# Optimization experiments

Measured on AMD Instinct MI355X. Metric: run time of the kernel, lower is better.

The kernel has to match this reference:

```python
import jax, jax.numpy as jnp
import numpy as np

NUM_GRAPHS = 64
N, E, H = 100000, 3200000, 64


def _glorot(k, shape):
    fan_in = shape[0]
    return jax.random.normal(k, shape, jnp.float32) * (1.0 / np.sqrt(fan_in))


def setup_inputs() -> dict:
    key = jax.random.key(0)
    ks = jax.random.split(key, 16)
    edge_index = jax.random.randint(ks[0], (2, E), 0, N)
    edge_weight = jax.random.uniform(ks[1], (E,), dtype=jnp.float32)
    batch = jnp.sort(jax.random.randint(ks[2], (N,), 0, NUM_GRAPHS))
    return {
        "edge_index": edge_index,
        "edge_weight": edge_weight,
        "batch": batch,
        "num_nodes": N,
        "W1": _glorot(ks[3], (1, H)), "b1": jnp.zeros((H,), jnp.float32),
        "W2": _glorot(ks[4], (H, H)), "b2": jnp.zeros((H,), jnp.float32),
        "W3": _glorot(ks[5], (H, H)), "b3": jnp.zeros((H,), jnp.float32),
        "W4": _glorot(ks[6], (H, H)), "b4": jnp.zeros((H,), jnp.float32),
        "W5": _glorot(ks[7], (H, H)), "b5": jnp.zeros((H,), jnp.float32),
        "lin_w": _glorot(ks[8], (H, 1)), "lin_b": jnp.zeros((1,), jnp.float32),
    }


def _gcn_layer(x, W, b, src, dst, w, n):
    # GCNConv(normalize=False): linear transform then weighted scatter-add over edges.
    h = x @ W                                  # [N, H]
    m = h[src] * w[:, None]                    # [E, H] messages
    return jax.ops.segment_sum(m, dst, num_segments=n) + b


def reference(edge_index, edge_weight, batch, num_nodes,
              W1, b1, W2, b2, W3, b3, W4, b4, W5, b5, lin_w, lin_b):
    src, dst = edge_index[0], edge_index[1]
    x = jnp.ones((num_nodes, 1), jnp.float32)
    for W, b in ((W1, b1), (W2, b2), (W3, b3), (W4, b4), (W5, b5)):
        x = jax.nn.relu(_gcn_layer(x, W, b, src, dst, edge_weight, num_nodes))
        # dropout p=0.1 is identity in eval mode
    # global mean pool per graph
    sums = jax.ops.segment_sum(x, batch, num_segments=NUM_GRAPHS)      # [G, H]
    counts = jax.ops.segment_sum(jnp.ones((num_nodes,), x.dtype), batch,
                                 num_segments=NUM_GRAPHS)
    pooled = sums / jnp.maximum(counts, 1.0)[:, None]
    return pooled @ lin_w + lin_b                                      # [G, 1]
```

## Files before the change

kernel.cpp:

```cpp
#include <hip/hip_runtime.h>

#define H 64
#define NUM_GRAPHS 64
#define BSHIFT 8
#define BSIZE 256
#define MAXNB 512
#define CHUNK 8192
#define RPB 16

typedef unsigned int uint;
typedef unsigned short ushort;
typedef __attribute__((ext_vector_type(4))) float f32x4;
typedef __attribute__((ext_vector_type(8))) short short8;

__device__ __forceinline__ float bf2f(ushort u) {
    return __uint_as_float(((uint)u) << 16);
}
__device__ __forceinline__ ushort f2bf(float f) {
    uint b = __float_as_uint(f);
    b += 0x7FFFu + ((b >> 16) & 1u);
    return (ushort)(b >> 16);
}

__global__ __launch_bounds__(1024) void bhist_kernel(const int* __restrict__ dst,
        int* __restrict__ bucketCnt, int E, int NB) {
    __shared__ int h[MAXNB];
    int tid = threadIdx.x;
    for (int i = tid; i < NB; i += 1024) h[i] = 0;
    __syncthreads();
    int base = blockIdx.x * CHUNK;
    int end = min(base + CHUNK, E);
    for (int e = base + tid; e < end; e += 1024)
        atomicAdd(&h[dst[e] >> BSHIFT], 1);
    __syncthreads();
    for (int i = tid; i < NB; i += 1024)
        if (h[i]) atomicAdd(&bucketCnt[i], h[i]);
}

__global__ __launch_bounds__(MAXNB) void bscan_kernel(const int* __restrict__ bucketCnt,
        int* __restrict__ bucketPtr, int* __restrict__ bucketCur, int NB) {
    __shared__ int s[MAXNB];
    int tid = threadIdx.x;
    int v = (tid < NB) ? bucketCnt[tid] : 0;
    s[tid] = v;
    __syncthreads();
    for (int off = 1; off < MAXNB; off <<= 1) {
        int t = (tid >= off) ? s[tid - off] : 0;
        __syncthreads();
        s[tid] += t;
        __syncthreads();
    }
    if (tid < NB) {
        bucketPtr[tid + 1] = s[tid];
        bucketCur[tid] = s[tid] - v;
    }
    if (tid == 0) bucketPtr[0] = 0;
}

__global__ __launch_bounds__(1024) void part_kernel(const int* __restrict__ src,
        const int* __restrict__ dst, const float* __restrict__ w,
        int* __restrict__ bucketCur, int2* __restrict__ bucketed, int E, int NB) {
    __shared__ int h[MAXNB];
    __shared__ int basev[MAXNB];
    int tid = threadIdx.x;
    for (int i = tid; i < NB; i += 1024) h[i] = 0;
    __syncthreads();
    int cbase = blockIdx.x * CHUNK;
    int cend = min(cbase + CHUNK, E);
    for (int e = cbase + tid; e < cend; e += 1024)
        atomicAdd(&h[dst[e] >> BSHIFT], 1);
    __syncthreads();
    for (int i = tid; i < NB; i += 1024) {
        int c = h[i];
        basev[i] = c ? atomicAdd(&bucketCur[i], c) : 0;
    }
    __syncthreads();
    for (int i = tid; i < NB; i += 1024) h[i] = 0;
    __syncthreads();
    for (int e = cbase + tid; e < cend; e += 1024) {
        int d = dst[e];
        int b = d >> BSHIFT;
        int slot = atomicAdd(&h[b], 1);
        bucketed[basev[b] + slot] =
            make_int2(((d & (BSIZE - 1)) << 17) | src[e], __float_as_int(w[e]));
    }
}

__global__ __launch_bounds__(512) void bsort_kernel(const int* __restrict__ bucketPtr,
        const int2* __restrict__ bucketed, uint* __restrict__ csr,
        int* __restrict__ rowptr, int N, int E) {
    __shared__ int cnt[BSIZE];
    __shared__ int pos[BSIZE];
    int b = blockIdx.x;
    int tid = threadIdx.x;
    int nodeBase = b << BSHIFT;
    int nNodes = min(BSIZE, N - nodeBase);
    if (tid < BSIZE) cnt[tid] = 0;
    __syncthreads();
    int ebeg = bucketPtr[b], eend = bucketPtr[b + 1];
    for (int e = ebeg + tid; e < eend; e += 512)
        atomicAdd(&cnt[bucketed[e].x >> 17], 1);
    __syncthreads();
    if (tid < BSIZE) pos[tid] = cnt[tid];
    __syncthreads();
    for (int off = 1; off < BSIZE; off <<= 1) {
        int t = (tid < BSIZE && tid >= off) ? pos[tid - off] : 0;
        __syncthreads();
        if (tid < BSIZE) pos[tid] += t;
        __syncthreads();
    }
    if (tid < nNodes)
        rowptr[nodeBase + tid] = ebeg + pos[tid] - cnt[tid];
    if (b == 0 && tid == 0) rowptr[N] = E;
    __syncthreads();
    if (tid < BSIZE) cnt[tid] = pos[tid] - cnt[tid];
    __syncthreads();
    for (int e = ebeg + tid; e < eend; e += 512) {
        int2 v = bucketed[e];
        int slot = atomicAdd(&cnt[v.x >> 17], 1);
        uint wb = (uint)v.y;
        wb += 0x7FFFu + ((wb >> 16) & 1u);
        uint w15 = (wb >> 16) & 0x7FFFu;
        uint s   = (uint)(v.x & 0x1FFFF);
        csr[ebeg + slot] = (s << 15) | w15;
    }
}

__global__ void layer1_kernel(const int* __restrict__ rowptr, const uint* __restrict__ csr,
                              const float* __restrict__ W1, const float* __restrict__ b1,
                              ushort* __restrict__ out, int N) {
    int lane = threadIdx.x & 63, wid = threadIdx.x >> 6;
    int row = blockIdx.x * 4 + wid;
    if (row >= N) return;
    int beg = rowptr[row], end = rowptr[row + 1];
    float s = 0.f;
    for (int e = beg + lane; e < end; e += 64) {
        uint p = __builtin_nontemporal_load(csr + e);
        s += __uint_as_float((p & 0x7FFFu) << 16);
    }
#pragma unroll
    for (int off = 32; off; off >>= 1) s += __shfl_xor(s, off);
    float v = s * W1[lane] + b1[lane];
    __builtin_nontemporal_store(f2bf(fmaxf(v, 0.f)), out + (size_t)row * H + lane);
}

__global__ __launch_bounds__(256) void layer_kernel(const int* __restrict__ rowptr,
        const uint* __restrict__ csr, const ushort* __restrict__ x,
        const float* __restrict__ W, const float* __restrict__ b,
        ushort* __restrict__ out, int N) {
    __shared__ alignas(16) ushort Wt[64][72];
    __shared__ alignas(16) ushort AG[RPB][72];
    int tid = threadIdx.x;
    for (int i = tid; i < 64 * 64; i += 256) {
        int k = i >> 6, c = i & 63;
        Wt[c][k] = f2bf(W[i]);
    }
    __syncthreads();
    int lane = tid & 63, wid = tid >> 6;
    int rowbase = blockIdx.x * RPB;
    for (int p = 0; p < 4; ++p) {
        int trow = wid * 4 + p;
        int row = rowbase + trow;
        float agg = 0.f;
        if (row < N) {
            int beg = rowptr[row], end = rowptr[row + 1];
            int len = end - beg;
            for (int ck = 0; ck < len; ck += 64) {
                uint pv = 0u;
                int idx = beg + ck + lane;
                if (idx < end) pv = __builtin_nontemporal_load(csr + idx);
                int rem = len - ck;
                int grps = rem >= 64 ? 8 : ((rem + 7) >> 3);
#pragma unroll
                for (int g = 0; g < 8; ++g) {
                    if (g < grps) {
#pragma unroll
                        for (int j = 0; j < 8; ++j) {
                            uint s = (uint)__builtin_amdgcn_readlane((int)pv, g * 8 + j);
                            float wf = __uint_as_float((s & 0x7FFFu) << 16);
                            float xv = bf2f(x[((s >> 15) << 6) + (uint)lane]);
                            agg = fmaf(wf, xv, agg);
                        }
                    }
                }
            }
        }
        AG[trow][lane] = f2bf(agg);
    }
    __syncthreads();
    int c0 = wid * 16;
    int cl = lane & 15, kg = lane >> 4;
    short8 a0 = *reinterpret_cast<const short8*>(&AG[cl][kg * 8]);
    short8 a1 = *reinterpret_cast<const short8*>(&AG[cl][32 + kg * 8]);
    short8 bb0 = *reinterpret_cast<const short8*>(&Wt[c0 + cl][kg * 8]);
    short8 bb1 = *reinterpret_cast<const short8*>(&Wt[c0 + cl][32 + kg * 8]);
    f32x4 acc = {0.f, 0.f, 0.f, 0.f};
    acc = __builtin_amdgcn_mfma_f32_16x16x32_bf16(a0, bb0, acc, 0, 0, 0);
    acc = __builtin_amdgcn_mfma_f32_16x16x32_bf16(a1, bb1, acc, 0, 0, 0);
    float bias = b[c0 + cl];
#pragma unroll
    for (int j = 0; j < 4; ++j) {
        int r = rowbase + kg * 4 + j;
        if (r < N) {
            float v = fmaxf(acc[j] + bias, 0.f);
            __builtin_nontemporal_store(f2bf(v), out + (size_t)r * H + c0 + cl);
        }
    }
}

__global__ void pool_kernel(const ushort* __restrict__ x, const int* __restrict__ batch,
                            const float* __restrict__ linw, float* __restrict__ gsum,
                            float* __restrict__ gcnt, int N) {
    __shared__ float bins[NUM_GRAPHS];
    __shared__ float cnts[NUM_GRAPHS];
    int tid = threadIdx.x;
    if (tid < NUM_GRAPHS) { bins[tid] = 0.f; cnts[tid] = 0.f; }
    __syncthreads();
    int node = blockIdx.x * 256 + tid;
    if (node < N) {
        const uint4* xv = reinterpret_cast<const uint4*>(x + (size_t)node * H);
        float acc = 0.f;
#pragma unroll
        for (int k = 0; k < 8; ++k) {
            uint4 u = xv[k];
            int c = k * 8;
            acc += bf2f((ushort)(u.x & 0xFFFF)) * linw[c + 0]
                 + bf2f((ushort)(u.x >> 16))    * linw[c + 1]
                 + bf2f((ushort)(u.y & 0xFFFF)) * linw[c + 2]
                 + bf2f((ushort)(u.y >> 16))    * linw[c + 3]
                 + bf2f((ushort)(u.z & 0xFFFF)) * linw[c + 4]
                 + bf2f((ushort)(u.z >> 16))    * linw[c + 5]
                 + bf2f((ushort)(u.w & 0xFFFF)) * linw[c + 6]
                 + bf2f((ushort)(u.w >> 16))    * linw[c + 7];
        }
        int g = batch[node];
        atomicAdd(&bins[g], acc);
        atomicAdd(&cnts[g], 1.f);
    }
    __syncthreads();
    if (tid < NUM_GRAPHS) {
        if (bins[tid] != 0.f || cnts[tid] != 0.f) {
            unsafeAtomicAdd(&gsum[tid], bins[tid]);
            unsafeAtomicAdd(&gcnt[tid], cnts[tid]);
        }
    }
}

__global__ void final_kernel(const float* __restrict__ gsum, const float* __restrict__ gcnt,
                             const float* __restrict__ lin_b, float* __restrict__ out) {
    int g = threadIdx.x;
    if (g < NUM_GRAPHS) out[g] = gsum[g] / fmaxf(gcnt[g], 1.f) + lin_b[0];
}

extern "C" void kernel_launch(void* const* d_in, const int* in_sizes, int n_in,
                              void* d_out, int out_size, void* d_ws, size_t ws_size,
                              hipStream_t stream) {
    const int*   edge_index = (const int*)d_in[0];
    const float* ew    = (const float*)d_in[1];
    const int*   batch = (const int*)d_in[2];
    const float* W1    = (const float*)d_in[4];
    const float* b1    = (const float*)d_in[5];
    const float* Wl[4] = {(const float*)d_in[6], (const float*)d_in[8],
                          (const float*)d_in[10], (const float*)d_in[12]};
    const float* bl[4] = {(const float*)d_in[7], (const float*)d_in[9],
                          (const float*)d_in[11], (const float*)d_in[13]};
    const float* linw  = (const float*)d_in[14];
    const float* linb  = (const float*)d_in[15];

    const int E = in_sizes[1];
    const int N = in_sizes[2];
    const int* src = edge_index;
    const int* dst = edge_index + E;
    const int NB = (N + BSIZE - 1) >> BSHIFT;

    char* base = (char*)d_ws;
    uint* csr = (uint*)base;
    size_t csrBytes = (((size_t)E * 4) + 255) & ~(size_t)255;
    ushort* bufA = (ushort*)(base + csrBytes);
    size_t featBytes = (size_t)N * H * 2;
    ushort* bufB = bufA + (size_t)N * H;
    int2* bucketed = (int2*)bufA;
    size_t span = 2 * featBytes;
    size_t bktBytes = (size_t)E * 8;
    if (bktBytes > span) span = bktBytes;
    span = (span + 255) & ~(size_t)255;
    char* tail = base + csrBytes + span;
    int* rowptr    = (int*)tail;
    int* bucketCnt = rowptr + (N + 1);
    int* bucketPtr = bucketCnt + MAXNB;
    int* bucketCur = bucketPtr + MAXNB + 1;
    float* gsum    = (float*)(bucketCur + MAXNB);
    float* gcnt    = gsum + NUM_GRAPHS;

    const int chunks = (E + CHUNK - 1) / CHUNK;

    hipMemsetAsync(bucketCnt, 0, MAXNB * sizeof(int), stream);
    bhist_kernel<<<chunks, 1024, 0, stream>>>(dst, bucketCnt, E, NB);
    bscan_kernel<<<1, MAXNB, 0, stream>>>(bucketCnt, bucketPtr, bucketCur, NB);
    part_kernel<<<chunks, 1024, 0, stream>>>(src, dst, ew, bucketCur, bucketed, E, NB);
    bsort_kernel<<<NB, 512, 0, stream>>>(bucketPtr, bucketed, csr, rowptr, N, E);

    layer1_kernel<<<(N + 3) / 4, 256, 0, stream>>>(rowptr, csr, W1, b1, bufA, N);

    ushort* in = bufA;
    ushort* outb = bufB;
    for (int l = 0; l < 4; ++l) {
        layer_kernel<<<(N + RPB - 1) / RPB, 256, 0, stream>>>(rowptr, csr, in, Wl[l], bl[l], outb, N);
        ushort* t = in; in = outb; outb = t;
    }

    hipMemsetAsync(gsum, 0, 2 * NUM_GRAPHS * sizeof(float), stream);
    pool_kernel<<<(N + 255) / 256, 256, 0, stream>>>(in, batch, linw, gsum, gcnt, N);
    final_kernel<<<1, 64, 0, stream>>>(gsum, gcnt, linb, (float*)d_out);
}
```

Before: 417.6 us.

## Sort edges by source within rows, fold degree into sort, fuse pooling into last layer

The bucket sort now uses a composite key of destination and high source bits, so edges within each row are ordered by source for better gather locality. It also accumulates per-node weighted degree, which turns layer 1 into an elementwise kernel instead of a CSR pass. Layer kernels become persistent with a fixed grid looping over row chunks. The last layer folds the ReLU output times lin_w straight into per-graph sums, so the final feature write and the pool kernel go away. The costs are larger shared memory in the sort, a longer prefix scan, and shared atomics in the last layer.

After: 552.9 us. 1.32x slower.

```diff
diff --git a/kernel.cpp b/kernel.cpp
--- a/kernel.cpp
+++ b/kernel.cpp
@@ -7,6 +7,9 @@
 #define MAXNB 512
 #define CHUNK 8192
 #define RPB 16
+#define NSB 64
+#define KEYS (BSIZE * NSB)
+#define GRID_L 1024
 
 typedef unsigned int uint;
 typedef unsigned short ushort;
@@ -88,161 +91,161 @@
 
 __global__ __launch_bounds__(512) void bsort_kernel(const int* __restrict__ bucketPtr,
         const int2* __restrict__ bucketed, uint* __restrict__ csr,
-        int* __restrict__ rowptr, int N, int E) {
-    __shared__ int cnt[BSIZE];
-    __shared__ int pos[BSIZE];
+        int* __restrict__ rowptr, float* __restrict__ degw, int N, int E) {
+    __shared__ int cnt[KEYS];
+    __shared__ int parts[512];
+    __shared__ float wsum[BSIZE];
     int b = blockIdx.x;
     int tid = threadIdx.x;
     int nodeBase = b << BSHIFT;
     int nNodes = min(BSIZE, N - nodeBase);
-    if (tid < BSIZE) cnt[tid] = 0;
+    for (int i = tid; i < KEYS; i += 512) cnt[i] = 0;
+    if (tid < BSIZE) wsum[tid] = 0.f;
     __syncthreads();
     int ebeg = bucketPtr[b], eend = bucketPtr[b + 1];
-    for (int e = ebeg + tid; e < eend; e += 512)
-        atomicAdd(&cnt[bucketed[e].x >> 17], 1);
-    __syncthreads();
-    if (tid < BSIZE) pos[tid] = cnt[tid];
-    __syncthreads();
-    for (int off = 1; off < BSIZE; off <<= 1) {
-        int t = (tid < BSIZE && tid >= off) ? pos[tid - off] : 0;
-        __syncthreads();
-        if (tid < BSIZE) pos[tid] += t;
-        __syncthreads();
-    }
-    if (tid < nNodes)
-        rowptr[nodeBase + tid] = ebeg + pos[tid] - cnt[tid];
-    if (b == 0 && tid == 0) rowptr[N] = E;
-    __syncthreads();
-    if (tid < BSIZE) cnt[tid] = pos[tid] - cnt[tid];
-    __syncthreads();
     for (int e = ebeg + tid; e < eend; e += 512) {
         int2 v = bucketed[e];
-        int slot = atomicAdd(&cnt[v.x >> 17], 1);
+        int key = ((v.x >> 17) << 6) | ((int)(((uint)(v.x & 0x1FFFF)) >> 11));
+        atomicAdd(&cnt[key], 1);
+    }
+    __syncthreads();
+    int base = tid * 32;
+    int run = 0;
+#pragma unroll
+    for (int j = 0; j < 32; ++j) { int t = cnt[base + j]; cnt[base + j] = run; run += t; }
+    parts[tid] = run;
+    __syncthreads();
+    for (int off = 1; off < 512; off <<= 1) {
+        int t = (tid >= off) ? parts[tid - off] : 0;
+        __syncthreads();
+        parts[tid] += t;
+        __syncthreads();
+    }
+    int add = (tid > 0) ? parts[tid - 1] : 0;
+#pragma unroll
+    for (int j = 0; j < 32; ++j) cnt[base + j] += add;
+    __syncthreads();
+    if (tid < nNodes) rowptr[nodeBase + tid] = ebeg + cnt[tid << 6];
+    if (b == 0 && tid == 0) rowptr[N] = E;
+    __syncthreads();
+    for (int e = ebeg + tid; e < eend; e += 512) {
+        int2 v = bucketed[e];
+        int dl = v.x >> 17;
+        int key = (dl << 6) | ((int)(((uint)(v.x & 0x1FFFF)) >> 11));
+        int slot = atomicAdd(&cnt[key], 1);
         uint wb = (uint)v.y;
         wb += 0x7FFFu + ((wb >> 16) & 1u);
         uint w15 = (wb >> 16) & 0x7FFFu;
-        uint s   = (uint)(v.x & 0x1FFFF);
-        csr[ebeg + slot] = (s << 15) | w15;
-    }
-}
-
-__global__ void layer1_kernel(const int* __restrict__ rowptr, const uint* __restrict__ csr,
-                              const float* __restrict__ W1, const float* __restrict__ b1,
-                              ushort* __restrict__ out, int N) {
-    int lane = threadIdx.x & 63, wid = threadIdx.x >> 6;
-    int row = blockIdx.x * 4 + wid;
-    if (row >= N) return;
-    int beg = rowptr[row], end = rowptr[row + 1];
-    float s = 0.f;
-    for (int e = beg + lane; e < end; e += 64) {
-        uint p = __builtin_nontemporal_load(csr + e);
-        s += __uint_as_float((p & 0x7FFFu) << 16);
-    }
-#pragma unroll
-    for (int off = 32; off; off >>= 1) s += __shfl_xor(s, off);
-    float v = s * W1[lane] + b1[lane];
-    __builtin_nontemporal_store(f2bf(fmaxf(v, 0.f)), out + (size_t)row * H + lane);
-}
-
+        csr[ebeg + slot] = (((uint)(v.x & 0x1FFFF)) << 15) | w15;
+        atomicAdd(&wsum[dl], __uint_as_float(w15 << 16));
+    }
+    __syncthreads();
+    if (tid < nNodes) degw[nodeBase + tid] = wsum[tid];
+}
+
+__global__ void layer1_kernel(const float* __restrict__ degw, const float* __restrict__ W1,
+                              const float* __restrict__ b1, ushort* __restrict__ out, int N) {
+    int gid = blockIdx.x * 256 + threadIdx.x;
+    if (gid >= N * 16) return;
+    int i = gid >> 4, c4 = (gid & 15) * 4;
+    float d = degw[i];
+    uint lo = (uint)f2bf(fmaxf(d * W1[c4 + 0] + b1[c4 + 0], 0.f))
+            | ((uint)f2bf(fmaxf(d * W1[c4 + 1] + b1[c4 + 1], 0.f)) << 16);
+    uint hi = (uint)f2bf(fmaxf(d * W1[c4 + 2] + b1[c4 + 2], 0.f))
+            | ((uint)f2bf(fmaxf(d * W1[c4 + 3] + b1[c4 + 3], 0.f)) << 16);
+    uint2 v = make_uint2(lo, hi);
+    *reinterpret_cast<uint2*>(out + ((size_t)i << 6) + c4) = v;
+}
+
+__global__ void count_kernel(const int* __restrict__ batch, float* __restrict__ gcnt, int N) {
+    __shared__ int bins[NUM_GRAPHS];
+    int tid = threadIdx.x;
+    if (tid < NUM_GRAPHS) bins[tid] = 0;
+    __syncthreads();
+    int node = blockIdx.x * 256 + tid;
+    if (node < N) atomicAdd(&bins[batch[node]], 1);
+    __syncthreads();
+    if (tid < NUM_GRAPHS && bins[tid])
+        unsafeAtomicAdd(&gcnt[tid], (float)bins[tid]);
+}
+
+template<bool LAST>
 __global__ __launch_bounds__(256) void layer_kernel(const int* __restrict__ rowptr,
         const uint* __restrict__ csr, const ushort* __restrict__ x,
-        const float* __restrict__ W, const float* __restrict__ b,
-        ushort* __restrict__ out, int N) {
+        const float* __restrict__ W, const float* __restrict__ bvec,
+        ushort* __restrict__ out, const int* __restrict__ batch,
+        const float* __restrict__ linw, float* __restrict__ gsum,
+        int N, int nchunk) {
     __shared__ alignas(16) ushort Wt[64][72];
     __shared__ alignas(16) ushort AG[RPB][72];
+    __shared__ float gbins[NUM_GRAPHS];
     int tid = threadIdx.x;
     for (int i = tid; i < 64 * 64; i += 256) {
         int k = i >> 6, c = i & 63;
         Wt[c][k] = f2bf(W[i]);
     }
+    if (LAST && tid < NUM_GRAPHS) gbins[tid] = 0.f;
     __syncthreads();
     int lane = tid & 63, wid = tid >> 6;
-    int rowbase = blockIdx.x * RPB;
-    for (int p = 0; p < 4; ++p) {
-        int trow = wid * 4 + p;
-        int row = rowbase + trow;
-        float agg = 0.f;
-        if (row < N) {
-            int beg = rowptr[row], end = rowptr[row + 1];
-            int len = end - beg;
-            for (int ck = 0; ck < len; ck += 64) {
-                uint pv = 0u;
-                int idx = beg + ck + lane;
-                if (idx < end) pv = __builtin_nontemporal_load(csr + idx);
-                int rem = len - ck;
-                int grps = rem >= 64 ? 8 : ((rem + 7) >> 3);
-#pragma unroll
-                for (int g = 0; g < 8; ++g) {
-                    if (g < grps) {
-#pragma unroll
-                        for (int j = 0; j < 8; ++j) {
-                            uint s = (uint)__builtin_amdgcn_readlane((int)pv, g * 8 + j);
-                            float wf = __uint_as_float((s & 0x7FFFu) << 16);
-                            float xv = bf2f(x[((s >> 15) << 6) + (uint)lane]);
-                            agg = fmaf(wf, xv, agg);
+    int cl = lane & 15, kg = lane >> 4;
+    for (int chunk = blockIdx.x; chunk < nchunk; chunk += GRID_L) {
+        int rowbase = chunk * RPB;
+        for (int p = 0; p < 4; ++p) {
+            int trow = wid * 4 + p;
+            int row = rowbase + trow;
+            float agg = 0.f;
+            if (row < N) {
+                int beg = rowptr[row], end = rowptr[row + 1];
+                int len = end - beg;
+                for (int ck = 0; ck < len; ck += 64) {
+                    uint pv = 0u;
+                    int idx = beg + ck + lane;
+                    if (idx < end) pv = __builtin_nontemporal_load(csr + idx);
+                    int rem = len - ck;
+                    int grps = rem >= 64 ? 8 : ((rem + 7) >> 3);
+#pragma unroll
+                    for (int g = 0; g < 8; ++g) {
+                        if (g < grps) {
+#pragma unroll
+                            for (int j = 0; j < 8; ++j) {
+                                uint s = (uint)__builtin_amdgcn_readlane((int)pv, g * 8 + j);
+                                float wf = __uint_as_float((s & 0x7FFFu) << 16);
+                                float xv = bf2f(x[((s >> 15) << 6) + (uint)lane]);
+                                agg = fmaf(wf, xv, agg);
+                            }
                         }
                     }
                 }
             }
+            AG[trow][lane] = f2bf(agg);
         }
-        AG[trow][lane] = f2bf(agg);
-    }
-    __syncthreads();
-    int c0 = wid * 16;
-    int cl = lane & 15, kg = lane >> 4;
-    short8 a0 = *reinterpret_cast<const short8*>(&AG[cl][kg * 8]);
-    short8 a1 = *reinterpret_cast<const short8*>(&AG[cl][32 + kg * 8]);
-    short8 bb0 = *reinterpret_cast<const short8*>(&Wt[c0 + cl][kg * 8]);
-    short8 bb1 = *reinterpret_cast<const short8*>(&Wt[c0 + cl][32 + kg * 8]);
-    f32x4 acc = {0.f, 0.f, 0.f, 0.f};
-    acc = __builtin_amdgcn_mfma_f32_16x16x32_bf16(a0, bb0, acc, 0, 0, 0);
-    acc = __builtin_amdgcn_mfma_f32_16x16x32_bf16(a1, bb1, acc, 0, 0, 0);
-    float bias = b[c0 + cl];
-#pragma unroll
-    for (int j = 0; j < 4; ++j) {
-        int r = rowbase + kg * 4 + j;
-        if (r < N) {
-            float v = fmaxf(acc[j] + bias, 0.f);
-            __builtin_nontemporal_store(f2bf(v), out + (size_t)r * H + c0 + cl);
+        __syncthreads();
+        int c0 = wid * 16;
+        short8 a0 = *reinterpret_cast<const short8*>(&AG[cl][kg * 8]);
+        short8 a1 = *reinterpret_cast<const short8*>(&AG[cl][32 + kg * 8]);
+        short8 bb0 = *reinterpret_cast<const short8*>(&Wt[c0 + cl][kg * 8]);
+        short8 bb1 = *reinterpret_cast<const short8*>(&Wt[c0 + cl][32 + kg * 8]);
+        f32x4 acc = {0.f, 0.f, 0.f, 0.f};
+        acc = __builtin_amdgcn_mfma_f32_16x16x32_bf16(a0, bb0, acc, 0, 0, 0);
+        acc = __builtin_amdgcn_mfma_f32_16x16x32_bf16(a1, bb1, acc, 0, 0, 0);
+        float bias = bvec[c0 + cl];
+        float lw = LAST ? linw[c0 + cl] : 0.f;
+#pragma unroll
+        for (int j = 0; j < 4; ++j) {
+            int r = rowbase + kg * 4 + j;
+            if (r < N) {
+                float v = fmaxf(acc[j] + bias, 0.f);
+                if (!LAST) {
+                    __builtin_nontemporal_store(f2bf(v), out + ((size_t)r << 6) + c0 + cl);
+                } else {
+                    atomicAdd(&gbins[batch[r]], v * lw);
+                }
+            }
         }
-    }
-}
-
-__global__ void pool_kernel(const ushort* __restrict__ x, const int* __restrict__ batch,
-                            const float* __restrict__ linw, float* __restrict__ gsum,
-                            float* __restrict__ gcnt, int N) {
-    __shared__ float bins[NUM_GRAPHS];
-    __shared__ float cnts[NUM_GRAPHS];
-    int tid = threadIdx.x;
-    if (tid < NUM_GRAPHS) { bins[tid] = 0.f; cnts[tid] = 0.f; }
-    __syncthreads();
-    int node = blockIdx.x * 256 + tid;
-    if (node < N) {
-        const uint4* xv = reinterpret_cast<const uint4*>(x + (size_t)node * H);
-        float acc = 0.f;
-#pragma unroll
-        for (int k = 0; k < 8; ++k) {
-            uint4 u = xv[k];
-            int c = k * 8;
-            acc += bf2f((ushort)(u.x & 0xFFFF)) * linw[c + 0]
-                 + bf2f((ushort)(u.x >> 16))    * linw[c + 1]
-                 + bf2f((ushort)(u.y & 0xFFFF)) * linw[c + 2]
-                 + bf2f((ushort)(u.y >> 16))    * linw[c + 3]
-                 + bf2f((ushort)(u.z & 0xFFFF)) * linw[c + 4]
-                 + bf2f((ushort)(u.z >> 16))    * linw[c + 5]
-                 + bf2f((ushort)(u.w & 0xFFFF)) * linw[c + 6]
-                 + bf2f((ushort)(u.w >> 16))    * linw[c + 7];
-        }
-        int g = batch[node];
-        atomicAdd(&bins[g], acc);
-        atomicAdd(&cnts[g], 1.f);
-    }
-    __syncthreads();
-    if (tid < NUM_GRAPHS) {
-        if (bins[tid] != 0.f || cnts[tid] != 0.f) {
-            unsafeAtomicAdd(&gsum[tid], bins[tid]);
-            unsafeAtomicAdd(&gcnt[tid], cnts[tid]);
-        }
+        __syncthreads();
+    }
+    if (LAST) {
+        if (tid < NUM_GRAPHS) unsafeAtomicAdd(&gsum[tid], gbins[tid]);
     }
 }
 
@@ -272,6 +275,7 @@
     const int* src = edge_index;
     const int* dst = edge_index + E;
     const int NB = (N + BSIZE - 1) >> BSHIFT;
+    const int nchunk = (N + RPB - 1) / RPB;
 
     char* base = (char*)d_ws;
     uint* csr = (uint*)base;
@@ -291,25 +295,29 @@
     int* bucketCur = bucketPtr + MAXNB + 1;
     float* gsum    = (float*)(bucketCur + MAXNB);
     float* gcnt    = gsum + NUM_GRAPHS;
+    float* degw    = gcnt + NUM_GRAPHS;
 
     const int chunks = (E + CHUNK - 1) / CHUNK;
 
     hipMemsetAsync(bucketCnt, 0, MAXNB * sizeof(int), stream);
+    hipMemsetAsync(gsum, 0, 2 * NUM_GRAPHS * sizeof(float), stream);
     bhist_kernel<<<chunks, 1024, 0, stream>>>(dst, bucketCnt, E, NB);
     bscan_kernel<<<1, MAXNB, 0, stream>>>(bucketCnt, bucketPtr, bucketCur, NB);
     part_kernel<<<chunks, 1024, 0, stream>>>(src, dst, ew, bucketCur, bucketed, E, NB);
-    bsort_kernel<<<NB, 512, 0, stream>>>(bucketPtr, bucketed, csr, rowptr, N, E);
-
-    layer1_kernel<<<(N + 3) / 4, 256, 0, stream>>>(rowptr, csr, W1, b1, bufA, N);
+    bsort_kernel<<<NB, 512, 0, stream>>>(bucketPtr, bucketed, csr, rowptr, degw, N, E);
+
+    layer1_kernel<<<(N * 16 + 255) / 256, 256, 0, stream>>>(degw, W1, b1, bufA, N);
+    count_kernel<<<(N + 255) / 256, 256, 0, stream>>>(batch, gcnt, N);
 
     ushort* in = bufA;
     ushort* outb = bufB;
-    for (int l = 0; l < 4; ++l) {
-        layer_kernel<<<(N + RPB - 1) / RPB, 256, 0, stream>>>(rowptr, csr, in, Wl[l], bl[l], outb, N);
+    for (int l = 0; l < 3; ++l) {
+        layer_kernel<false><<<GRID_L, 256, 0, stream>>>(rowptr, csr, in, Wl[l], bl[l],
+                outb, batch, linw, gsum, N, nchunk);
         ushort* t = in; in = outb; outb = t;
     }
-
-    hipMemsetAsync(gsum, 0, 2 * NUM_GRAPHS * sizeof(float), stream);
-    pool_kernel<<<(N + 255) / 256, 256, 0, stream>>>(in, batch, linw, gsum, gcnt, N);
+    layer_kernel<true><<<GRID_L, 256, 0, stream>>>(rowptr, csr, in, Wl[3], bl[3],
+            outb, batch, linw, gsum, N, nchunk);
+
     final_kernel<<<1, 64, 0, stream>>>(gsum, gcnt, linb, (float*)d_out);
 }
```
